# Kernel tuning notes

Hardware: AMD Instinct MI355X
Metric: run time of the kernel (lower is better)

## Reference

```python
import jax, jax.numpy as jnp
import numpy as np

B, T, C = 8, 4096, 512


def setup_inputs() -> dict:
    key = jax.random.key(0)
    k1, k2, k3 = jax.random.split(key, 3)
    inputs = jax.random.normal(k1, (B, T, C), dtype=jnp.float32)
    # stable-ish recurrence: |A| < 1
    A_real = jax.random.uniform(k2, (C,), dtype=jnp.float32, minval=0.5, maxval=0.99)
    A_imag = jax.random.uniform(k3, (C,), dtype=jnp.float32, minval=-0.1, maxval=0.1)
    h0_real = jnp.zeros((B, C), dtype=jnp.float32)
    h0_imag = jnp.zeros((B, C), dtype=jnp.float32)
    return {"inputs": inputs, "A_real": A_real, "A_imag": A_imag,
            "h0_real": h0_real, "h0_imag": h0_imag}


def reference(inputs, A_real, A_imag, h0_real, h0_imag):
    # Diagonal complex linear recurrence:
    #   h[t] = A * h[t-1] + x[t]   (x real, added to real part only)
    # Output: states at every step, stacked (real, imag) -> (B, T, C, 2)
    def step(carry, x_t):
        hr, hi = carry
        nr = hr * A_real - hi * A_imag + x_t
        ni = A_imag * hr + A_real * hi
        return (nr, ni), (nr, ni)

    xs = jnp.swapaxes(inputs, 0, 1)  # (T, B, C)
    _, (real_seq, imag_seq) = jax.lax.scan(step, (h0_real, h0_imag), xs)
    real_seq = jnp.swapaxes(real_seq, 0, 1)  # (B, T, C)
    imag_seq = jnp.swapaxes(imag_seq, 0, 1)
    return jnp.stack([real_seq, imag_seq], axis=-1)  # (B, T, C, 2)
```

## Files before the change

### kernel.cpp

```cpp
#include <hip/hip_runtime.h>

#define BB 8
#define TT 4096
#define CC 512
#define NCHUNK 128
#define LCHUNK (TT / NCHUNK)

__global__ __launch_bounds__(256) void rec_pass1(const float* __restrict__ x,
                                                 const float* __restrict__ Ar,
                                                 const float* __restrict__ Ai,
                                                 float2* __restrict__ s_end) {
    const int tid   = threadIdx.x;
    const int blk   = blockIdx.x;
    const int b     = blk / NCHUNK;
    const int chunk = blk % NCHUNK;
    const int t0    = chunk * LCHUNK;

    const float2 a_r = ((const float2*)Ar)[tid];
    const float2 a_i = ((const float2*)Ai)[tid];

    const float2* xp = (const float2*)(x + (size_t)(b * TT + t0) * CC) + tid;

    float hr0 = 0.f, hi0 = 0.f, hr1 = 0.f, hi1 = 0.f;
#pragma unroll 8
    for (int t = 0; t < LCHUNK; ++t) {
        float2 xv = xp[(size_t)t * (CC / 2)];
        float nr0 = fmaf(hr0, a_r.x, fmaf(-hi0, a_i.x, xv.x));
        float ni0 = fmaf(a_i.x, hr0, a_r.x * hi0);
        float nr1 = fmaf(hr1, a_r.y, fmaf(-hi1, a_i.y, xv.y));
        float ni1 = fmaf(a_i.y, hr1, a_r.y * hi1);
        hr0 = nr0; hi0 = ni0; hr1 = nr1; hi1 = ni1;
    }
    float4* sp = (float4*)(s_end + (size_t)(chunk * BB + b) * CC);
    sp[tid] = make_float4(hr0, hi0, hr1, hi1);
}

__global__ __launch_bounds__(256) void rec_pass2(const float* __restrict__ Ar,
                                                 const float* __restrict__ Ai,
                                                 const float* __restrict__ h0r,
                                                 const float* __restrict__ h0i,
                                                 const float2* __restrict__ s_end,
                                                 float2* __restrict__ h_start) {
    const int gid = blockIdx.x * 256 + threadIdx.x;
    const int b = gid / CC;
    const int c = gid % CC;

    float ar = Ar[c], ai = Ai[c];
    float pr = ar, pi = ai;
#pragma unroll
    for (int s = 0; s < 5; ++s) {
        float nr = pr * pr - pi * pi;
        float ni = 2.f * pr * pi;
        pr = nr; pi = ni;
    }

    float hr = h0r[gid], hi = h0i[gid];
#pragma unroll 4
    for (int j = 0; j < NCHUNK; ++j) {
        h_start[(size_t)(j * BB + b) * CC + c] = make_float2(hr, hi);
        float2 s = s_end[(size_t)(j * BB + b) * CC + c];
        float nr = pr * hr - pi * hi + s.x;
        float ni = pi * hr + pr * hi + s.y;
        hr = nr; hi = ni;
    }
}

__global__ __launch_bounds__(256) void rec_pass3(const float* __restrict__ x,
                                                 const float* __restrict__ Ar,
                                                 const float* __restrict__ Ai,
                                                 const float2* __restrict__ h_start,
                                                 float4* __restrict__ out) {
    const int tid   = threadIdx.x;
    const int blk   = blockIdx.x;
    const int b     = blk / NCHUNK;
    const int chunk = blk % NCHUNK;
    const int t0    = chunk * LCHUNK;

    const float2 a_r = ((const float2*)Ar)[tid];
    const float2 a_i = ((const float2*)Ai)[tid];

    const float2* xp = (const float2*)(x + (size_t)(b * TT + t0) * CC) + tid;
    const float4* hs = (const float4*)(h_start + (size_t)(chunk * BB + b) * CC);
    float4 h = hs[tid];
    float hr0 = h.x, hi0 = h.y, hr1 = h.z, hi1 = h.w;

    float4* op = out + (size_t)(b * TT + t0) * (CC / 2) + tid;
#pragma unroll 8
    for (int t = 0; t < LCHUNK; ++t) {
        float2 xv = xp[(size_t)t * (CC / 2)];
        float nr0 = fmaf(hr0, a_r.x, fmaf(-hi0, a_i.x, xv.x));
        float ni0 = fmaf(a_i.x, hr0, a_r.x * hi0);
        float nr1 = fmaf(hr1, a_r.y, fmaf(-hi1, a_i.y, xv.y));
        float ni1 = fmaf(a_i.y, hr1, a_r.y * hi1);
        hr0 = nr0; hi0 = ni0; hr1 = nr1; hi1 = ni1;
        op[(size_t)t * (CC / 2)] = make_float4(nr0, ni0, nr1, ni1);
    }
}

extern "C" void kernel_launch(void* const* d_in, const int* in_sizes, int n_in,
                              void* d_out, int out_size, void* d_ws, size_t ws_size,
                              hipStream_t stream) {
    const float* x   = (const float*)d_in[0];
    const float* Ar  = (const float*)d_in[1];
    const float* Ai  = (const float*)d_in[2];
    const float* h0r = (const float*)d_in[3];
    const float* h0i = (const float*)d_in[4];
    float* out = (float*)d_out;

    float2* s_end   = (float2*)d_ws;
    float2* h_start = s_end + (size_t)NCHUNK * BB * CC;

    rec_pass1<<<BB * NCHUNK, 256, 0, stream>>>(x, Ar, Ai, s_end);
    rec_pass2<<<(BB * CC) / 256, 256, 0, stream>>>(Ar, Ai, h0r, h0i, s_end, h_start);
    rec_pass3<<<BB * NCHUNK, 256, 0, stream>>>(x, Ar, Ai, h_start, (float4*)out);
}
```

Measured before the change: 211.8 us.

## Fold chunk-carry scan into emit kernel, removing serial middle pass

```diff
diff --git a/kernel.cpp b/kernel.cpp
--- a/kernel.cpp
+++ b/kernel.cpp
@@ -6,10 +6,10 @@
 #define NCHUNK 128
 #define LCHUNK (TT / NCHUNK)
 
-__global__ __launch_bounds__(256) void rec_pass1(const float* __restrict__ x,
-                                                 const float* __restrict__ Ar,
-                                                 const float* __restrict__ Ai,
-                                                 float2* __restrict__ s_end) {
+__global__ __launch_bounds__(256, 4) void rec_ends(const float* __restrict__ x,
+                                                   const float* __restrict__ Ar,
+                                                   const float* __restrict__ Ai,
+                                                   float4* __restrict__ s_end) {
     const int tid   = threadIdx.x;
     const int blk   = blockIdx.x;
     const int b     = blk / NCHUNK;
@@ -31,45 +31,16 @@
         float ni1 = fmaf(a_i.y, hr1, a_r.y * hi1);
         hr0 = nr0; hi0 = ni0; hr1 = nr1; hi1 = ni1;
     }
-    float4* sp = (float4*)(s_end + (size_t)(chunk * BB + b) * CC);
-    sp[tid] = make_float4(hr0, hi0, hr1, hi1);
+    s_end[(size_t)(chunk * BB + b) * (CC / 2) + tid] = make_float4(hr0, hi0, hr1, hi1);
 }
 
-__global__ __launch_bounds__(256) void rec_pass2(const float* __restrict__ Ar,
-                                                 const float* __restrict__ Ai,
-                                                 const float* __restrict__ h0r,
-                                                 const float* __restrict__ h0i,
-                                                 const float2* __restrict__ s_end,
-                                                 float2* __restrict__ h_start) {
-    const int gid = blockIdx.x * 256 + threadIdx.x;
-    const int b = gid / CC;
-    const int c = gid % CC;
-
-    float ar = Ar[c], ai = Ai[c];
-    float pr = ar, pi = ai;
-#pragma unroll
-    for (int s = 0; s < 5; ++s) {
-        float nr = pr * pr - pi * pi;
-        float ni = 2.f * pr * pi;
-        pr = nr; pi = ni;
-    }
-
-    float hr = h0r[gid], hi = h0i[gid];
-#pragma unroll 4
-    for (int j = 0; j < NCHUNK; ++j) {
-        h_start[(size_t)(j * BB + b) * CC + c] = make_float2(hr, hi);
-        float2 s = s_end[(size_t)(j * BB + b) * CC + c];
-        float nr = pr * hr - pi * hi + s.x;
-        float ni = pi * hr + pr * hi + s.y;
-        hr = nr; hi = ni;
-    }
-}
-
-__global__ __launch_bounds__(256) void rec_pass3(const float* __restrict__ x,
-                                                 const float* __restrict__ Ar,
-                                                 const float* __restrict__ Ai,
-                                                 const float2* __restrict__ h_start,
-                                                 float4* __restrict__ out) {
+__global__ __launch_bounds__(256, 4) void rec_emit(const float* __restrict__ x,
+                                                   const float* __restrict__ Ar,
+                                                   const float* __restrict__ Ai,
+                                                   const float* __restrict__ h0r,
+                                                   const float* __restrict__ h0i,
+                                                   const float4* __restrict__ s_end,
+                                                   float4* __restrict__ out) {
     const int tid   = threadIdx.x;
     const int blk   = blockIdx.x;
     const int b     = blk / NCHUNK;
@@ -79,11 +50,30 @@
     const float2 a_r = ((const float2*)Ar)[tid];
     const float2 a_i = ((const float2*)Ai)[tid];
 
+    float p0r = a_r.x, p0i = a_i.x, p1r = a_r.y, p1i = a_i.y;
+#pragma unroll
+    for (int s = 0; s < 5; ++s) {
+        float n0r = p0r * p0r - p0i * p0i, n0i = 2.f * p0r * p0i;
+        float n1r = p1r * p1r - p1i * p1i, n1i = 2.f * p1r * p1i;
+        p0r = n0r; p0i = n0i; p1r = n1r; p1i = n1i;
+    }
+
+    float2 h0rv = ((const float2*)(h0r + (size_t)b * CC))[tid];
+    float2 h0iv = ((const float2*)(h0i + (size_t)b * CC))[tid];
+    float hr0 = h0rv.x, hr1 = h0rv.y, hi0 = h0iv.x, hi1 = h0iv.y;
+
+    const float4* sp = s_end + tid;
+#pragma unroll 4
+    for (int j = 0; j < chunk; ++j) {
+        float4 s = sp[(size_t)(j * BB + b) * (CC / 2)];
+        float nr0 = p0r * hr0 - p0i * hi0 + s.x;
+        float ni0 = p0i * hr0 + p0r * hi0 + s.y;
+        float nr1 = p1r * hr1 - p1i * hi1 + s.z;
+        float ni1 = p1i * hr1 + p1r * hi1 + s.w;
+        hr0 = nr0; hi0 = ni0; hr1 = nr1; hi1 = ni1;
+    }
+
     const float2* xp = (const float2*)(x + (size_t)(b * TT + t0) * CC) + tid;
-    const float4* hs = (const float4*)(h_start + (size_t)(chunk * BB + b) * CC);
-    float4 h = hs[tid];
-    float hr0 = h.x, hi0 = h.y, hr1 = h.z, hi1 = h.w;
-
     float4* op = out + (size_t)(b * TT + t0) * (CC / 2) + tid;
 #pragma unroll 8
     for (int t = 0; t < LCHUNK; ++t) {
@@ -107,10 +97,8 @@
     const float* h0i = (const float*)d_in[4];
     float* out = (float*)d_out;
 
-    float2* s_end   = (float2*)d_ws;
-    float2* h_start = s_end + (size_t)NCHUNK * BB * CC;
+    float4* s_end = (float4*)d_ws;
 
-    rec_pass1<<<BB * NCHUNK, 256, 0, stream>>>(x, Ar, Ai, s_end);
-    rec_pass2<<<(BB * CC) / 256, 256, 0, stream>>>(Ar, Ai, h0r, h0i, s_end, h_start);
-    rec_pass3<<<BB * NCHUNK, 256, 0, stream>>>(x, Ar, Ai, h_start, (float4*)out);
+    rec_ends<<<BB * NCHUNK, 256, 0, stream>>>(x, Ar, Ai, s_end);
+    rec_emit<<<BB * NCHUNK, 256, 0, stream>>>(x, Ar, Ai, h0r, h0i, s_end, (float4*)out);
 }
```

New measurement: 207.0 us. 1.02x faster.
